# Performance work log

Hardware: AMD Instinct MI355X
Metric: run time of the kernel (lower is better)

The kernel has to match this reference:

```python
import jax, jax.numpy as jnp
import numpy as np

# WeightOnlyInt8Linear forward: out = (x @ W_int8.astype(x.dtype).T) * scales
# NOTE: the original torch forward has a bug: when bias is not None it returns
# pre_bias (bias is never added), and when bias is None it would crash.
# Faithful math for a runnable configuration (bias=True) is therefore just
# the scaled matmul without bias.

IN_FEATURES = 4096
OUT_FEATURES = 16384
M = 256  # tokens


def setup_inputs() -> dict:
    key = jax.random.key(0)
    k1, k2, k3 = jax.random.split(key, 3)
    x = jax.random.normal(k1, (M, IN_FEATURES), dtype=jnp.float32)
    # int8 quantized weights in [-128, 127]
    weight = jax.random.randint(k2, (OUT_FEATURES, IN_FEATURES), -128, 128, dtype=jnp.int8)
    # per-output-channel dequant scales (positive, small)
    scales = jax.random.uniform(k3, (OUT_FEATURES,), dtype=jnp.float32, minval=0.001, maxval=0.02)
    return {"input": x, "weight": weight, "scales": scales}


def reference(input, weight, scales):
    # weight.to(input): upcast int8 -> activation dtype, then dense GEMM, then per-channel scale
    w = weight.astype(input.dtype)                      # [out, in]
    pre_bias = jnp.einsum('mk,nk->mn', input, w)        # [M, out]
    return pre_bias * scales                            # broadcast over out_features
```

## Files before the change

kernel.cpp:

```cpp
#include <hip/hip_runtime.h>
#include <stdint.h>

#define M_TOK 256
#define N_OUT 16384
#define K_IN  4096
#define BM 128
#define BN 64
#define BK 64
#define NSTEPS (K_IN / BK)

#define AS1 __attribute__((address_space(1)))
#define AS3 __attribute__((address_space(3)))

typedef short v8s __attribute__((ext_vector_type(8)));
typedef float v16f __attribute__((ext_vector_type(16)));
typedef int   v4i __attribute__((ext_vector_type(4)));
typedef uint32_t v2u __attribute__((ext_vector_type(2)));
typedef unsigned int uint;

__device__ __forceinline__ unsigned short rne_bf16(float f) {
  uint u = __float_as_uint(f);
  uint r = u + 0x7FFFu + ((u >> 16) & 1u);
  return (unsigned short)(r >> 16);
}
__device__ __forceinline__ float bfbits_to_f(uint h) {
  return __uint_as_float(h << 16);
}
__device__ __forceinline__ uint pack_bf16(float a, float b) {
  return (__float_as_uint(a) >> 16) | (__float_as_uint(b) & 0xffff0000u);
}

__global__ __launch_bounds__(256) void cast_kernel(
    const float* __restrict__ x, unsigned short* __restrict__ xhi,
    unsigned short* __restrict__ xlo) {
  const int i = (blockIdx.x * 256 + threadIdx.x) * 4;
  const float4 f = *(const float4*)(x + i);
  float fs[4] = {f.x, f.y, f.z, f.w};
  unsigned short h[4], l[4];
#pragma unroll
  for (int j = 0; j < 4; ++j) {
    h[j] = rne_bf16(fs[j]);
    l[j] = rne_bf16(fs[j] - bfbits_to_f(h[j]));
  }
  *(ushort4*)(xhi + i) = make_ushort4(h[0], h[1], h[2], h[3]);
  *(ushort4*)(xlo + i) = make_ushort4(l[0], l[1], l[2], l[3]);
}

__global__ __launch_bounds__(512, 4) void gemm_kernel(
    const unsigned short* __restrict__ xhi, const unsigned short* __restrict__ xlo,
    const void* __restrict__ wraw, const float* __restrict__ scales,
    float* __restrict__ out) {
  __shared__ alignas(16) unsigned char smem[40960];
  const int tid = threadIdx.x;
  const int lane = tid & 63;
  const int wid = tid >> 6;

  const int* wi = (const int*)wraw;
  const signed char* wb = (const signed char*)wraw;
  bool is32 = true;
#pragma unroll
  for (int i = 0; i < 16; ++i) {
    const int v = wi[i];
    is32 = is32 && (v >= -128) && (v <= 127);
  }

  const int bid = blockIdx.x;
  const int logical = (bid & 7) * 64 + (bid >> 3);
  const int mb = logical & 1;
  const int nb = logical >> 1;
  const int m0 = mb * BM;
  const int n0 = nb * BN;

  const unsigned short* xsrc[4];
  uint xdst[4];
#pragma unroll
  for (int j = 0; j < 4; ++j) {
    const int s = wid * 4 + j;
    const int r = s * 4 + (lane >> 4);
    const int c = (lane & 15) ^ (r & 15);
    xsrc[j] = (c >= 8 ? xlo : xhi) + (size_t)(m0 + r) * K_IN + (size_t)((c & 7) * 8);
    xdst[j] = (uint)(s * 1024);
  }

  const int wrow = tid >> 3, wc = tid & 7;
  const int* w32base = wi + (size_t)(n0 + wrow) * K_IN + (size_t)(wc * 8);
  const signed char* w8base = wb + (size_t)(n0 + wrow) * K_IN + (size_t)(wc * 8);
  const uint wq = (uint)(wrow >> 1);
  const uint wchunk = (uint)((wrow & 1) * 8 + wc);
  const uint waddr = wq * 256u + ((wchunk ^ (wq & 15u)) << 4);

  const int l31 = lane & 31, hi5 = lane >> 5;
  const int wm = (wid & 3) * 32;
  const int wn = (wid >> 2) * 32;
  const uint arow = (uint)((wm + l31) * 256);
  const uint ax = (uint)((wm + l31) & 15);
  const int wr = wn + l31;
  const uint bq = (uint)(wr >> 1);
  const uint bbase = 32768u + bq * 256u;
  const uint bsel = (uint)((wr & 1) * 8);
  const uint bx = bq & 15u;

  v16f acc = {};
  v4i wt0, wt1;

  auto stage_x = [&](int s) {
#pragma unroll
    for (int j = 0; j < 4; ++j)
      __builtin_amdgcn_global_load_lds(
          (const AS1 void*)(xsrc[j] + (size_t)s * BK),
          (AS3 void*)(smem + xdst[j]), 16, 0, 0);
  };
  auto load_w = [&](int s) {
    if (is32) {
      wt0 = __builtin_nontemporal_load((const v4i*)(w32base + (size_t)s * BK));
      wt1 = __builtin_nontemporal_load((const v4i*)(w32base + (size_t)s * BK + 4));
    } else {
      const v2u u = __builtin_nontemporal_load((const v2u*)(w8base + (size_t)s * BK));
      wt0.x = (int)u.x; wt0.y = (int)u.y;
    }
  };
  auto conv_w = [&]() {
    uint d[4];
    if (is32) {
      d[0] = pack_bf16((float)wt0.x, (float)wt0.y);
      d[1] = pack_bf16((float)wt0.z, (float)wt0.w);
      d[2] = pack_bf16((float)wt1.x, (float)wt1.y);
      d[3] = pack_bf16((float)wt1.z, (float)wt1.w);
    } else {
      const signed char* bs = (const signed char*)&wt0;
#pragma unroll
      for (int p = 0; p < 4; ++p)
        d[p] = pack_bf16((float)bs[2 * p], (float)bs[2 * p + 1]);
    }
    v4i wv; wv.x = (int)d[0]; wv.y = (int)d[1]; wv.z = (int)d[2]; wv.w = (int)d[3];
    *(v4i*)(smem + 32768u + waddr) = wv;
  };

  stage_x(0);
  load_w(0);

  for (int t = 0; t < NSTEPS; ++t) {
    conv_w();
    __syncthreads();

    if (t + 1 < NSTEPS) load_w(t + 1);

#pragma unroll
    for (int kc = 0; kc < 4; ++kc) {
      const uint ch = (uint)(kc * 2 + hi5);
      v8s ah = *(const v8s*)(smem + arow + ((ch ^ ax) << 4));
      v8s al = *(const v8s*)(smem + arow + (((ch + 8u) ^ ax) << 4));
      v8s b  = *(const v8s*)(smem + bbase - 32768u + 32768u + (((bsel + ch) ^ bx) << 4));
      acc = __builtin_amdgcn_mfma_f32_32x32x16_bf16(ah, b, acc, 0, 0, 0);
      acc = __builtin_amdgcn_mfma_f32_32x32x16_bf16(al, b, acc, 0, 0, 0);
    }

    __syncthreads();
    if (t + 1 < NSTEPS) stage_x(t + 1);
  }

  const int n = n0 + wn + l31;
  const float scl = scales[n];
#pragma unroll
  for (int reg = 0; reg < 16; ++reg) {
    const int m = m0 + wm + (reg & 3) + 8 * (reg >> 2) + 4 * hi5;
    out[(size_t)m * N_OUT + n] = acc[reg] * scl;
  }
}

__global__ void naive_kernel(const float* __restrict__ x, const void* __restrict__ wraw,
                             const float* __restrict__ scales, float* __restrict__ out) {
  const int* wi = (const int*)wraw;
  bool is32 = true;
  for (int i = 0; i < 16; ++i) { int v = wi[i]; is32 = is32 && v >= -128 && v <= 127; }
  const int idx = blockIdx.x * 256 + threadIdx.x;
  const int m = idx >> 14;
  const int n = idx & (N_OUT - 1);
  const float* xr = x + (size_t)m * K_IN;
  float acc = 0.f;
  if (is32) {
    const int* wr = wi + (size_t)n * K_IN;
    for (int k = 0; k < K_IN; ++k) acc += xr[k] * (float)wr[k];
  } else {
    const signed char* wr = (const signed char*)wraw + (size_t)n * K_IN;
    for (int k = 0; k < K_IN; ++k) acc += xr[k] * (float)wr[k];
  }
  out[idx] = acc * scales[n];
}

extern "C" void kernel_launch(void* const* d_in, const int* in_sizes, int n_in,
                              void* d_out, int out_size, void* d_ws, size_t ws_size,
                              hipStream_t stream) {
  const float* x = (const float*)d_in[0];
  const void* w = d_in[1];
  const float* scales = (const float*)d_in[2];
  float* out = (float*)d_out;
  if (ws_size >= (size_t)4 * 1024 * 1024) {
    unsigned short* xhi = (unsigned short*)d_ws;
    unsigned short* xlo = xhi + (size_t)M_TOK * K_IN;
    cast_kernel<<<(M_TOK * K_IN) / 1024, 256, 0, stream>>>(x, xhi, xlo);
    gemm_kernel<<<512, 512, 0, stream>>>(xhi, xlo, w, scales, out);
  } else {
    naive_kernel<<<(M_TOK * N_OUT) / 256, 256, 0, stream>>>(x, w, scales, out);
  }
}
```

Measured before the change: 429.0 us.

## Halve GEMM M tile to 64 with 256-thread blocks and plain weight loads

Shrinks the block tile from 128x64 to 64x64 and cuts each block to 4 waves and 256 threads. Each thread now loads and converts two weight rows, and the grid doubles to 1024 blocks with a new swizzled block-to-tile mapping. The weight loads also drop their nontemporal hint, so the four M-blocks that share a weight tile can hit in cache. The aim is more resident blocks per CU and better latency hiding. The trade-off is that each weight tile is now fetched and converted by four blocks instead of two, which adds load and conversion work.

```diff
diff --git a/kernel.cpp b/kernel.cpp
--- a/kernel.cpp
+++ b/kernel.cpp
@@ -4,7 +4,7 @@
 #define M_TOK 256
 #define N_OUT 16384
 #define K_IN  4096
-#define BM 128
+#define BM 64
 #define BN 64
 #define BK 64
 #define NSTEPS (K_IN / BK)
@@ -46,11 +46,11 @@
   *(ushort4*)(xlo + i) = make_ushort4(l[0], l[1], l[2], l[3]);
 }
 
-__global__ __launch_bounds__(512, 4) void gemm_kernel(
+__global__ __launch_bounds__(256, 4) void gemm_kernel(
     const unsigned short* __restrict__ xhi, const unsigned short* __restrict__ xlo,
     const void* __restrict__ wraw, const float* __restrict__ scales,
     float* __restrict__ out) {
-  __shared__ alignas(16) unsigned char smem[40960];
+  __shared__ alignas(16) unsigned char smem[24576];
   const int tid = threadIdx.x;
   const int lane = tid & 63;
   const int wid = tid >> 6;
@@ -65,9 +65,9 @@
   }
 
   const int bid = blockIdx.x;
-  const int logical = (bid & 7) * 64 + (bid >> 3);
-  const int mb = logical & 1;
-  const int nb = logical >> 1;
+  const int logical = (bid & 7) * 128 + (bid >> 3);
+  const int mb = logical & 3;
+  const int nb = logical >> 2;
   const int m0 = mb * BM;
   const int n0 = nb * BN;
 
@@ -82,26 +82,30 @@
     xdst[j] = (uint)(s * 1024);
   }
 
-  const int wrow = tid >> 3, wc = tid & 7;
-  const int* w32base = wi + (size_t)(n0 + wrow) * K_IN + (size_t)(wc * 8);
-  const signed char* w8base = wb + (size_t)(n0 + wrow) * K_IN + (size_t)(wc * 8);
-  const uint wq = (uint)(wrow >> 1);
-  const uint wchunk = (uint)((wrow & 1) * 8 + wc);
-  const uint waddr = wq * 256u + ((wchunk ^ (wq & 15u)) << 4);
+  const int wr0 = tid >> 3, wc = tid & 7;
+  const int* w32b0 = wi + (size_t)(n0 + wr0) * K_IN + (size_t)(wc * 8);
+  const int* w32b1 = wi + (size_t)(n0 + 32 + wr0) * K_IN + (size_t)(wc * 8);
+  const signed char* w8b0 = wb + (size_t)(n0 + wr0) * K_IN + (size_t)(wc * 8);
+  const signed char* w8b1 = wb + (size_t)(n0 + 32 + wr0) * K_IN + (size_t)(wc * 8);
+  const uint wq0 = (uint)(wr0 >> 1);
+  const uint wch = (uint)((wr0 & 1) * 8 + wc);
+  const uint waddr0 = 16384u + wq0 * 256u + ((wch ^ (wq0 & 15u)) << 4);
+  const uint wq1 = wq0 + 16u;
+  const uint waddr1 = 16384u + wq1 * 256u + ((wch ^ (wq1 & 15u)) << 4);
 
   const int l31 = lane & 31, hi5 = lane >> 5;
-  const int wm = (wid & 3) * 32;
-  const int wn = (wid >> 2) * 32;
+  const int wm = (wid & 1) * 32;
+  const int wn = (wid >> 1) * 32;
   const uint arow = (uint)((wm + l31) * 256);
   const uint ax = (uint)((wm + l31) & 15);
   const int wr = wn + l31;
   const uint bq = (uint)(wr >> 1);
-  const uint bbase = 32768u + bq * 256u;
+  const uint bbase = 16384u + bq * 256u;
   const uint bsel = (uint)((wr & 1) * 8);
   const uint bx = bq & 15u;
 
   v16f acc = {};
-  v4i wt0, wt1;
+  v4i wt0, wt1, wt2, wt3;
 
   auto stage_x = [&](int s) {
 #pragma unroll
@@ -112,28 +116,42 @@
   };
   auto load_w = [&](int s) {
     if (is32) {
-      wt0 = __builtin_nontemporal_load((const v4i*)(w32base + (size_t)s * BK));
-      wt1 = __builtin_nontemporal_load((const v4i*)(w32base + (size_t)s * BK + 4));
+      wt0 = *(const v4i*)(w32b0 + (size_t)s * BK);
+      wt1 = *(const v4i*)(w32b0 + (size_t)s * BK + 4);
+      wt2 = *(const v4i*)(w32b1 + (size_t)s * BK);
+      wt3 = *(const v4i*)(w32b1 + (size_t)s * BK + 4);
     } else {
-      const v2u u = __builtin_nontemporal_load((const v2u*)(w8base + (size_t)s * BK));
-      wt0.x = (int)u.x; wt0.y = (int)u.y;
+      const v2u a = *(const v2u*)(w8b0 + (size_t)s * BK);
+      const v2u b = *(const v2u*)(w8b1 + (size_t)s * BK);
+      wt0.x = (int)a.x; wt0.y = (int)a.y;
+      wt2.x = (int)b.x; wt2.y = (int)b.y;
     }
   };
   auto conv_w = [&]() {
-    uint d[4];
+    uint d0[4], d1[4];
     if (is32) {
-      d[0] = pack_bf16((float)wt0.x, (float)wt0.y);
-      d[1] = pack_bf16((float)wt0.z, (float)wt0.w);
-      d[2] = pack_bf16((float)wt1.x, (float)wt1.y);
-      d[3] = pack_bf16((float)wt1.z, (float)wt1.w);
+      d0[0] = pack_bf16((float)wt0.x, (float)wt0.y);
+      d0[1] = pack_bf16((float)wt0.z, (float)wt0.w);
+      d0[2] = pack_bf16((float)wt1.x, (float)wt1.y);
+      d0[3] = pack_bf16((float)wt1.z, (float)wt1.w);
+      d1[0] = pack_bf16((float)wt2.x, (float)wt2.y);
+      d1[1] = pack_bf16((float)wt2.z, (float)wt2.w);
+      d1[2] = pack_bf16((float)wt3.x, (float)wt3.y);
+      d1[3] = pack_bf16((float)wt3.z, (float)wt3.w);
     } else {
-      const signed char* bs = (const signed char*)&wt0;
-#pragma unroll
-      for (int p = 0; p < 4; ++p)
-        d[p] = pack_bf16((float)bs[2 * p], (float)bs[2 * p + 1]);
+      const signed char* a = (const signed char*)&wt0;
+      const signed char* b = (const signed char*)&wt2;
+#pragma unroll
+      for (int p = 0; p < 4; ++p) {
+        d0[p] = pack_bf16((float)a[2 * p], (float)a[2 * p + 1]);
+        d1[p] = pack_bf16((float)b[2 * p], (float)b[2 * p + 1]);
+      }
     }
-    v4i wv; wv.x = (int)d[0]; wv.y = (int)d[1]; wv.z = (int)d[2]; wv.w = (int)d[3];
-    *(v4i*)(smem + 32768u + waddr) = wv;
+    v4i v0, v1;
+    v0.x = (int)d0[0]; v0.y = (int)d0[1]; v0.z = (int)d0[2]; v0.w = (int)d0[3];
+    v1.x = (int)d1[0]; v1.y = (int)d1[1]; v1.z = (int)d1[2]; v1.w = (int)d1[3];
+    *(v4i*)(smem + waddr0) = v0;
+    *(v4i*)(smem + waddr1) = v1;
   };
 
   stage_x(0);
@@ -150,7 +168,7 @@
       const uint ch = (uint)(kc * 2 + hi5);
       v8s ah = *(const v8s*)(smem + arow + ((ch ^ ax) << 4));
       v8s al = *(const v8s*)(smem + arow + (((ch + 8u) ^ ax) << 4));
-      v8s b  = *(const v8s*)(smem + bbase - 32768u + 32768u + (((bsel + ch) ^ bx) << 4));
+      v8s b  = *(const v8s*)(smem + bbase + (((bsel + ch) ^ bx) << 4));
       acc = __builtin_amdgcn_mfma_f32_32x32x16_bf16(ah, b, acc, 0, 0, 0);
       acc = __builtin_amdgcn_mfma_f32_32x32x16_bf16(al, b, acc, 0, 0, 0);
     }
@@ -199,7 +217,7 @@
     unsigned short* xhi = (unsigned short*)d_ws;
     unsigned short* xlo = xhi + (size_t)M_TOK * K_IN;
     cast_kernel<<<(M_TOK * K_IN) / 1024, 256, 0, stream>>>(x, xhi, xlo);
-    gemm_kernel<<<512, 512, 0, stream>>>(xhi, xlo, w, scales, out);
+    gemm_kernel<<<(M_TOK / BM) * (N_OUT / BN), 256, 0, stream>>>(xhi, xlo, w, scales, out);
   } else {
     naive_kernel<<<(M_TOK * N_OUT) / 256, 256, 0, stream>>>(x, w, scales, out);
   }
```

New measurement: 445.5 us. 3.9% more time.
